# Kernel tuning notes

Hardware: AMD Instinct MI355X
Metric: run time of the kernel (lower is better)

Reference implementation:

```python
import jax, jax.numpy as jnp
import numpy as np

N_VERTS = 1_000_000
N_JOINTS = 55  # SMPL-X: NUM_JOINTS + 1


def setup_inputs() -> dict:
    key = jax.random.key(0)
    k1, k2, k3 = jax.random.split(key, 3)
    points = jax.random.normal(k1, (N_VERTS, 3), dtype=jnp.float32)
    w = jax.random.uniform(k2, (N_VERTS, N_JOINTS), dtype=jnp.float32)
    weights = w / jnp.sum(w, axis=-1, keepdims=True)  # LBS weights sum to 1 per vertex
    SE3 = jax.random.normal(k3, (N_JOINTS, 4, 4), dtype=jnp.float32)
    return {"points": points, "weights": weights, "SE3": SE3}


def reference(points, weights, SE3):
    # RigidTransform.weight: blend per-joint SE(3) matrices with per-vertex weights
    # weights: [N, J], SE3: [J, 4, 4] -> A: [N, 4, 4]
    A = jnp.einsum('nj,jkl->nkl', weights, SE3)
    R = A[:, :3, :3]  # [N, 3, 3]
    T = A[:, :3, 3]   # [N, 3]
    # RigidTransform._transform_points: R @ p + T
    return jnp.einsum('nkl,nl->nk', R, points) + T
```

## Files before the change

kernel.cpp:

```cpp
#include <hip/hip_runtime.h>

#define NJ  55
#define BLK 64
#define SLAB (BLK * NJ)

__global__ __launch_bounds__(BLK) void lbs_kernel(
    const float* __restrict__ points,
    const float* __restrict__ weights,
    const float* __restrict__ se3,
    float* __restrict__ out,
    int n_verts)
{
    __shared__ __align__(16) float s_w[SLAB];

    const int lane = threadIdx.x;
    const int row0 = blockIdx.x * BLK;

    if (row0 + BLK <= n_verts) {
        const float4* src = (const float4*)(weights + (size_t)row0 * NJ);
        float4* dst = (float4*)s_w;
        #pragma unroll
        for (int i = 0; i < SLAB / 4 / BLK; ++i)
            dst[lane + i * BLK] = src[lane + i * BLK];
        const int tail = SLAB / 4 - (SLAB / 4 / BLK) * BLK;
        if (lane < tail)
            dst[lane + (SLAB / 4 / BLK) * BLK] = src[lane + (SLAB / 4 / BLK) * BLK];
    } else {
        const int total = (n_verts - row0) * NJ;
        const float* src = weights + (size_t)row0 * NJ;
        for (int i = lane; i < total; i += BLK) s_w[i] = src[i];
    }
    __builtin_amdgcn_s_waitcnt(0);

    const int n = row0 + lane;
    if (n >= n_verts) return;

    float a[12];
    #pragma unroll
    for (int e = 0; e < 12; ++e) a[e] = 0.f;

    const float* wr = &s_w[lane * NJ];
    const float4* M = (const float4*)se3;

    #pragma unroll 5
    for (int j = 0; j < NJ; ++j) {
        const float w = wr[j];
        const float4 r0 = M[j * 4 + 0];
        const float4 r1 = M[j * 4 + 1];
        const float4 r2 = M[j * 4 + 2];
        a[0] += w * r0.x; a[1] += w * r0.y; a[2]  += w * r0.z; a[3]  += w * r0.w;
        a[4] += w * r1.x; a[5] += w * r1.y; a[6]  += w * r1.z; a[7]  += w * r1.w;
        a[8] += w * r2.x; a[9] += w * r2.y; a[10] += w * r2.z; a[11] += w * r2.w;
    }

    const float px = points[n * 3 + 0];
    const float py = points[n * 3 + 1];
    const float pz = points[n * 3 + 2];

    out[n * 3 + 0] = a[0] * px + a[1] * py + a[2]  * pz + a[3];
    out[n * 3 + 1] = a[4] * px + a[5] * py + a[6]  * pz + a[7];
    out[n * 3 + 2] = a[8] * px + a[9] * py + a[10] * pz + a[11];
}

extern "C" void kernel_launch(void* const* d_in, const int* in_sizes, int n_in,
                              void* d_out, int out_size, void* d_ws, size_t ws_size,
                              hipStream_t stream) {
    const float* points  = (const float*)d_in[0];
    const float* weights = (const float*)d_in[1];
    const float* se3     = (const float*)d_in[2];
    float* out = (float*)d_out;

    const int n_verts = in_sizes[0] / 3;
    const int grid = (n_verts + BLK - 1) / BLK;
    lbs_kernel<<<grid, BLK, 0, stream>>>(points, weights, se3, out, n_verts);
}
```

Baseline: 317.2 us.

## Use persistent blocks with register-staged prefetch of the next weight slab

Switches to a persistent grid of a fixed number of single-wave blocks that stride over vertex slabs. Each iteration issues global loads of the next slab's weights into registers while computing the current slab from LDS, then writes them to LDS. The aim is to hide global memory latency behind compute. In exchange it costs extra registers (limited by the launch-bounds occupancy hint) and fixes the grid size to a hard-coded value.

```diff
diff --git a/kernel.cpp b/kernel.cpp
--- a/kernel.cpp
+++ b/kernel.cpp
@@ -1,65 +1,101 @@
 #include <hip/hip_runtime.h>
 
-#define NJ  55
-#define BLK 64
-#define SLAB (BLK * NJ)
+#define NJ   55
+#define BLK  64
+#define SLABF (BLK * NJ)
+#define STG  14
 
-__global__ __launch_bounds__(BLK) void lbs_kernel(
+__global__ __launch_bounds__(BLK, 3) void lbs_kernel(
     const float* __restrict__ points,
     const float* __restrict__ weights,
     const float* __restrict__ se3,
     float* __restrict__ out,
-    int n_verts)
+    int n_verts, int n_slabs, int gstride)
 {
-    __shared__ __align__(16) float s_w[SLAB];
+    __shared__ __align__(16) float s_w[SLABF];
+    const int lane = threadIdx.x;
 
-    const int lane = threadIdx.x;
-    const int row0 = blockIdx.x * BLK;
+    int s = blockIdx.x;
+    if (s >= n_slabs) return;
 
-    if (row0 + BLK <= n_verts) {
-        const float4* src = (const float4*)(weights + (size_t)row0 * NJ);
-        float4* dst = (float4*)s_w;
-        #pragma unroll
-        for (int i = 0; i < SLAB / 4 / BLK; ++i)
-            dst[lane + i * BLK] = src[lane + i * BLK];
-        const int tail = SLAB / 4 - (SLAB / 4 / BLK) * BLK;
-        if (lane < tail)
-            dst[lane + (SLAB / 4 / BLK) * BLK] = src[lane + (SLAB / 4 / BLK) * BLK];
-    } else {
-        const int total = (n_verts - row0) * NJ;
-        const float* src = weights + (size_t)row0 * NJ;
-        for (int i = lane; i < total; i += BLK) s_w[i] = src[i];
-    }
-    __builtin_amdgcn_s_waitcnt(0);
-
-    const int n = row0 + lane;
-    if (n >= n_verts) return;
-
-    float a[12];
-    #pragma unroll
-    for (int e = 0; e < 12; ++e) a[e] = 0.f;
-
-    const float* wr = &s_w[lane * NJ];
-    const float4* M = (const float4*)se3;
-
-    #pragma unroll 5
-    for (int j = 0; j < NJ; ++j) {
-        const float w = wr[j];
-        const float4 r0 = M[j * 4 + 0];
-        const float4 r1 = M[j * 4 + 1];
-        const float4 r2 = M[j * 4 + 2];
-        a[0] += w * r0.x; a[1] += w * r0.y; a[2]  += w * r0.z; a[3]  += w * r0.w;
-        a[4] += w * r1.x; a[5] += w * r1.y; a[6]  += w * r1.z; a[7]  += w * r1.w;
-        a[8] += w * r2.x; a[9] += w * r2.y; a[10] += w * r2.z; a[11] += w * r2.w;
+    {
+        const int rows = min(BLK, n_verts - s * BLK);
+        if (rows == BLK) {
+            const float4* src = (const float4*)(weights + (size_t)s * SLABF);
+            float4* dst = (float4*)s_w;
+            #pragma unroll
+            for (int i = 0; i < STG - 1; ++i) dst[lane + i * BLK] = src[lane + i * BLK];
+            if (lane < 48) dst[lane + (STG - 1) * BLK] = src[lane + (STG - 1) * BLK];
+        } else {
+            const float* src = weights + (size_t)s * SLABF;
+            for (int i = lane; i < rows * NJ; i += BLK) s_w[i] = src[i];
+        }
     }
 
-    const float px = points[n * 3 + 0];
-    const float py = points[n * 3 + 1];
-    const float pz = points[n * 3 + 2];
+    for (;;) {
+        const int snext = s + gstride;
+        const bool have_next = (snext < n_slabs);
 
-    out[n * 3 + 0] = a[0] * px + a[1] * py + a[2]  * pz + a[3];
-    out[n * 3 + 1] = a[4] * px + a[5] * py + a[6]  * pz + a[7];
-    out[n * 3 + 2] = a[8] * px + a[9] * py + a[10] * pz + a[11];
+        const int n = s * BLK + lane;
+        const bool act = (n < n_verts);
+        const int nc = act ? n : (n_verts - 1);
+
+        const float px = points[nc * 3 + 0];
+        const float py = points[nc * 3 + 1];
+        const float pz = points[nc * 3 + 2];
+
+        float4 stg[STG];
+        bool full_next = false;
+        if (have_next) {
+            const int rows = min(BLK, n_verts - snext * BLK);
+            full_next = (rows == BLK);
+            if (full_next) {
+                const float4* src = (const float4*)(weights + (size_t)snext * SLABF);
+                #pragma unroll
+                for (int i = 0; i < STG - 1; ++i) stg[i] = src[lane + i * BLK];
+                if (lane < 48) stg[STG - 1] = src[lane + (STG - 1) * BLK];
+            }
+        }
+
+        float a[12];
+        #pragma unroll
+        for (int e = 0; e < 12; ++e) a[e] = 0.f;
+
+        const float* wr = &s_w[lane * NJ];
+        const float4* M = (const float4*)se3;
+
+        #pragma unroll 5
+        for (int j = 0; j < NJ; ++j) {
+            const float w = wr[j];
+            const float4 r0 = M[j * 4 + 0];
+            const float4 r1 = M[j * 4 + 1];
+            const float4 r2 = M[j * 4 + 2];
+            a[0] += w * r0.x; a[1] += w * r0.y; a[2]  += w * r0.z; a[3]  += w * r0.w;
+            a[4] += w * r1.x; a[5] += w * r1.y; a[6]  += w * r1.z; a[7]  += w * r1.w;
+            a[8] += w * r2.x; a[9] += w * r2.y; a[10] += w * r2.z; a[11] += w * r2.w;
+        }
+
+        if (act) {
+            float* po = out + (size_t)n * 3;
+            po[0] = a[0] * px + a[1] * py + a[2]  * pz + a[3];
+            po[1] = a[4] * px + a[5] * py + a[6]  * pz + a[7];
+            po[2] = a[8] * px + a[9] * py + a[10] * pz + a[11];
+        }
+
+        if (!have_next) return;
+
+        if (full_next) {
+            float4* dst = (float4*)s_w;
+            #pragma unroll
+            for (int i = 0; i < STG - 1; ++i) dst[lane + i * BLK] = stg[i];
+            if (lane < 48) dst[lane + (STG - 1) * BLK] = stg[STG - 1];
+        } else {
+            const int rows = n_verts - snext * BLK;
+            const float* src = weights + (size_t)snext * SLABF;
+            for (int i = lane; i < rows * NJ; i += BLK) s_w[i] = src[i];
+        }
+        s = snext;
+    }
 }
 
 extern "C" void kernel_launch(void* const* d_in, const int* in_sizes, int n_in,
@@ -71,6 +107,9 @@
     float* out = (float*)d_out;
 
     const int n_verts = in_sizes[0] / 3;
-    const int grid = (n_verts + BLK - 1) / BLK;
-    lbs_kernel<<<grid, BLK, 0, stream>>>(points, weights, se3, out, n_verts);
+    const int n_slabs = (n_verts + BLK - 1) / BLK;
+    int grid = 11 * 256;
+    if (grid > n_slabs) grid = n_slabs;
+    lbs_kernel<<<grid, BLK, 0, stream>>>(points, weights, se3, out,
+                                         n_verts, n_slabs, grid);
 }
```

Result: slower. 359.6 us (+13.4%).
